# Kernel optimization log

Hardware: AMD Instinct MI355X
Metric: run time of the kernel (lower is better)

The kernel has to match this reference:

```python
import jax, jax.numpy as jnp
import numpy as np

T, B, D, H, OUT = 128, 256, 512, 768, 60


def setup_inputs() -> dict:
    key = jax.random.key(0)
    ks = jax.random.split(key, 8)
    def xavier(k, shape):
        fan_out, fan_in = shape
        limit = np.sqrt(6.0 / (fan_in + fan_out))
        return jax.random.uniform(k, shape, jnp.float32, -limit, limit)
    inp = {
        "input_sample": jax.random.normal(ks[0], (T, B, D), jnp.float32),
        # PyTorch LSTMCell params: weight_ih (4H, D), weight_hh (4H, H), biases (4H,)
        "W_ih": xavier(ks[1], (4 * H, D)),
        "W_hh": xavier(ks[2], (4 * H, H)),
        "b_ih": jax.random.uniform(ks[3], (4 * H,), jnp.float32, -1 / np.sqrt(H), 1 / np.sqrt(H)),
        "b_hh": jax.random.uniform(ks[4], (4 * H,), jnp.float32, -1 / np.sqrt(H), 1 / np.sqrt(H)),
        "W_fc": xavier(ks[5], (OUT, H)),
        "b_fc": jnp.zeros((OUT,), jnp.float32),
    }
    return inp


def _lstm_head(input_sample, W_ih, W_hh, b_ih, b_hh, W_fc, b_fc):
    B_ = input_sample.shape[1]
    H_ = W_hh.shape[1]
    # Precompute input projections for all time steps in one GEMM: (T, B, 4H)
    x_proj = jnp.einsum("tbd,gd->tbg", input_sample, W_ih) + b_ih + b_hh

    def step(carry, xp_t):
        h, c = carry
        gates = xp_t + h @ W_hh.T  # (B, 4H)
        i, f, g, o = jnp.split(gates, 4, axis=-1)  # PyTorch gate order: i, f, g, o
        i = jax.nn.sigmoid(i)
        f = jax.nn.sigmoid(f)
        g = jnp.tanh(g)
        o = jax.nn.sigmoid(o)
        c_new = f * c + i * g
        h_new = o * jnp.tanh(c_new)
        return (h_new, c_new), None

    h0 = jnp.zeros((B_, H_), input_sample.dtype)
    c0 = jnp.zeros((B_, H_), input_sample.dtype)
    (h_T, _), _ = jax.lax.scan(step, (h0, c0), x_proj)
    return h_T @ W_fc.T + b_fc  # (B, OUT)


def reference(input_sample, W_ih, W_hh, b_ih, b_hh, W_fc, b_fc):
    return _lstm_head(input_sample, W_ih, W_hh, b_ih, b_hh, W_fc, b_fc)
```

## Files before the change

kernel.cpp:

```cpp
#include <hip/hip_runtime.h>
#include <stdint.h>

#define T_ 128
#define B_ 256
#define D_ 512
#define H_ 768
#define NG 3072
#define OUT_ 60

using bf16x8 = __attribute__((ext_vector_type(8))) __bf16;
using f32x4  = __attribute__((ext_vector_type(4))) float;
using u32x4  = __attribute__((ext_vector_type(4))) unsigned int;

#define OFF_XB   ((size_t)0)
#define OFF_WI   (OFF_XB + (size_t)T_*B_*D_*2)
#define OFF_WHPK (OFF_WI + (size_t)NG*D_*2)
#define OFF_H    (OFF_WHPK + (size_t)NG*H_*2)
#define OFF_HT   (OFF_H + (size_t)2*B_*H_*2)
#define OFF_BAR  (OFF_HT + (size_t)B_*H_*4)
#define OFF_XP   (OFF_BAR + 65536)
#define OFF_END  (OFF_XP + (size_t)T_*B_*NG*2)

__device__ __forceinline__ unsigned short f2bf(float f) {
  union { float f; unsigned u; } v; v.f = f;
  unsigned r = (v.u + 0x7fffu + ((v.u >> 16) & 1u)) >> 16;
  return (unsigned short)r;
}
__device__ __forceinline__ float sigf(float x) {
  return __builtin_amdgcn_rcpf(1.0f + __expf(-x));
}
__device__ __forceinline__ float tanhf_(float x) {
  return 2.0f * __builtin_amdgcn_rcpf(1.0f + __expf(-2.0f * x)) - 1.0f;
}
__device__ __forceinline__ void gload16(const void* g, void* l) {
  __builtin_amdgcn_global_load_lds(
      (const __attribute__((address_space(1))) unsigned int*)g,
      (__attribute__((address_space(3))) unsigned int*)l, 16, 0, 0);
}
template<int OFF, bool SC1>
__device__ __forceinline__ u32x4 ld16(const void* p) {
  u32x4 r;
  if constexpr (SC1)
    asm volatile("global_load_dwordx4 %0, %1, off offset:%c2 sc0 sc1"
                 : "=v"(r) : "v"(p), "i"(OFF) : "memory");
  else
    asm volatile("global_load_dwordx4 %0, %1, off offset:%c2 sc0"
                 : "=v"(r) : "v"(p), "i"(OFF) : "memory");
  return r;
}
__device__ __forceinline__ unsigned ld4coh(const unsigned* p) {
  unsigned r;
  asm volatile("global_load_dword %0, %1, off sc0 sc1\n\ts_waitcnt vmcnt(0)"
               : "=v"(r) : "v"(p) : "memory");
  return r;
}
template<bool SC1>
__device__ __forceinline__ void st2(ushort* p, unsigned v) {
  if constexpr (SC1)
    asm volatile("global_store_short %0, %1, off sc0 sc1" :: "v"(p), "v"(v) : "memory");
  else
    asm volatile("global_store_short %0, %1, off sc0" :: "v"(p), "v"(v) : "memory");
}
__device__ __forceinline__ void st4coh(unsigned* p, unsigned v) {
  asm volatile("global_store_dword %0, %1, off sc0 sc1" :: "v"(p), "v"(v) : "memory");
}

__global__ void prep_kernel(const float* __restrict__ x,
                            const float* __restrict__ wihf,
                            const float* __restrict__ whhf,
                            uint8_t* __restrict__ ws) {
  ushort* xb = (ushort*)(ws + OFF_XB);
  ushort* wi = (ushort*)(ws + OFF_WI);
  ushort* whpk = (ushort*)(ws + OFF_WHPK);
  unsigned* bar = (unsigned*)(ws + OFF_BAR);
  const size_t tid = (size_t)blockIdx.x * blockDim.x + threadIdx.x;
  const size_t nth = (size_t)gridDim.x * blockDim.x;

  for (size_t i = tid; i < (size_t)T_*B_*D_/4; i += nth) {
    float4 v = ((const float4*)x)[i];
    ushort4 o; o.x=f2bf(v.x); o.y=f2bf(v.y); o.z=f2bf(v.z); o.w=f2bf(v.w);
    ((ushort4*)xb)[i] = o;
  }
  for (size_t i = tid; i < (size_t)NG*D_/4; i += nth) {
    float4 v = ((const float4*)wihf)[i];
    ushort4 o; o.x=f2bf(v.x); o.y=f2bf(v.y); o.z=f2bf(v.z); o.w=f2bf(v.w);
    ((ushort4*)wi)[i] = o;
  }
  for (size_t c = tid; c < (size_t)294912; c += nth) {
    const unsigned L = (unsigned)c & 63u;
    const unsigned r1 = (unsigned)(c >> 6);
    const unsigned nt = r1 % 6u, r2 = r1 / 6u;
    const unsigned kf = r2 % 24u, s = r2 / 24u;
    const unsigned i = nt*16u + (L & 15u);
    const unsigned G = (i & 3u)*768u + s*24u + (i >> 2);
    const unsigned k0 = kf*32u + (L >> 4)*8u;
    const float4 v0 = *(const float4*)(whhf + (size_t)G*768u + k0);
    const float4 v1 = *(const float4*)(whhf + (size_t)G*768u + k0 + 4);
    ushort4 o0, o1;
    o0.x=f2bf(v0.x); o0.y=f2bf(v0.y); o0.z=f2bf(v0.z); o0.w=f2bf(v0.w);
    o1.x=f2bf(v1.x); o1.y=f2bf(v1.y); o1.z=f2bf(v1.z); o1.w=f2bf(v1.w);
    *(ushort4*)(whpk + c*8)     = o0;
    *(ushort4*)(whpk + c*8 + 4) = o1;
  }
  for (size_t i = tid; i < 16384; i += nth) st4coh(&bar[i], 0u);
}

__global__ __launch_bounds__(256) void xproj_kernel(uint8_t* __restrict__ ws) {
  const ushort* __restrict__ xb = (const ushort*)(ws + OFF_XB);
  const ushort* __restrict__ wi = (const ushort*)(ws + OFF_WI);
  ushort* __restrict__ xp = (ushort*)(ws + OFF_XP);

  __shared__ ushort smA[128*64];
  __shared__ ushort smB[128*64];

  const int tid = threadIdx.x;
  const int lane = tid & 63;
  const int w = tid >> 6;
  const int bn = blockIdx.x % 24;
  const int bm = blockIdx.x / 24;
  const int m0 = bm * 128, n0 = bn * 128;
  const int mi = (w >> 1) * 64, ni = (w & 1) * 64;

  f32x4 acc[4][4] = {};

  for (int k0 = 0; k0 < D_; k0 += 64) {
    __syncthreads();
    #pragma unroll
    for (int i = 0; i < 4; ++i) {
      const int ig = w*4 + i;
      const int o  = ig*1024 + lane*16;
      const int row = o >> 7;
      const int colB = o & 127;
      const int scol = colB ^ ((row & 7) << 4);
      gload16((const uint8_t*)xb + ((size_t)(m0+row)*D_ + k0)*2 + scol,
              (uint8_t*)smA + ig*1024);
      gload16((const uint8_t*)wi + ((size_t)(n0+row)*D_ + k0)*2 + scol,
              (uint8_t*)smB + ig*1024);
    }
    __syncthreads();
    #pragma unroll
    for (int kk = 0; kk < 2; ++kk) {
      const int colB = kk*64 + (lane >> 4)*16;
      bf16x8 a[4], b[4];
      #pragma unroll
      for (int mt = 0; mt < 4; ++mt) {
        const int row = mi + mt*16 + (lane & 15);
        a[mt] = *(const bf16x8*)((const uint8_t*)smA + row*128 + (colB ^ ((row & 7) << 4)));
      }
      #pragma unroll
      for (int nt = 0; nt < 4; ++nt) {
        const int row = ni + nt*16 + (lane & 15);
        b[nt] = *(const bf16x8*)((const uint8_t*)smB + row*128 + (colB ^ ((row & 7) << 4)));
      }
      #pragma unroll
      for (int mt = 0; mt < 4; ++mt)
        #pragma unroll
        for (int nt = 0; nt < 4; ++nt)
          acc[mt][nt] = __builtin_amdgcn_mfma_f32_16x16x32_bf16(a[mt], b[nt], acc[mt][nt], 0, 0, 0);
    }
  }
  #pragma unroll
  for (int mt = 0; mt < 4; ++mt)
    #pragma unroll
    for (int nt = 0; nt < 4; ++nt) {
      const int r0 = m0 + mi + mt*16 + (lane >> 4)*4;
      const int c  = n0 + ni + nt*16 + (lane & 15);
      #pragma unroll
      for (int r = 0; r < 4; ++r)
        xp[(size_t)(r0 + r)*NG + c] = f2bf(acc[mt][nt][r]);
    }
}

template<bool SC1>
__device__ __forceinline__ void run_loop(uint8_t* ws, const ushort* whh_lds, float* gbuf,
                                         const float* bih, const float* bhh,
                                         int tid, int g, int s) {
  const int lane = tid & 63, w = tid >> 6, wq = w & 1, wm = w >> 1;
  const int l15 = lane & 15, hi = lane >> 4;
  ushort* hb = (ushort*)(ws + OFF_H);
  const ushort* xp = (const ushort*)(ws + OFF_XP);
  float* hT = (float*)(ws + OFF_HT);
  unsigned* bar = (unsigned*)(ws + OFF_BAR);
  float* gw = gbuf + w*816;

  float bias[3][4];
  #pragma unroll
  for (int j = 0; j < 3; ++j) {
    const int col = s*24 + wq*12 + hi + 4*j;
    #pragma unroll
    for (int q = 0; q < 4; ++q) bias[j][q] = bih[q*H_ + col] + bhh[q*H_ + col];
  }
  const int pl = (lane < 32) ? lane : 31;
  const unsigned* fp = bar + (size_t)(g*32 + pl) * 16;

  const ushort* xpb = xp + (size_t)(g*32 + wm*16 + l15)*NG + s*24 + wq*12 + hi;
  ushort xq[12];
  {
    const ushort* p = xpb;
    #pragma unroll
    for (int q = 0; q < 4; ++q)
      #pragma unroll
      for (int j = 0; j < 3; ++j)
        xq[q*3+j] = p[q*768 + 4*j];
  }

  float cc[3] = {0.f, 0.f, 0.f};

  #pragma unroll 1
  for (int t = 0; t < T_; ++t) {
    f32x4 acc[3] = {};
    if (t > 0) {
      while (1) {
        const unsigned v = ld4coh(fp);
        if (__all((int)(v >= (unsigned)t))) break;
        __builtin_amdgcn_s_sleep(1);
      }
      const ushort* hr = hb + ((size_t)(t & 1)*8 + g)*((size_t)32*H_)
                         + (size_t)(wm*16 + l15)*H_ + hi*8;
      u32x4 ah[24];
      #define LH(i) ah[i] = ld16<(i)*64, SC1>(hr)
      LH(0); LH(1); LH(2); LH(3); LH(4); LH(5); LH(6); LH(7);
      LH(8); LH(9); LH(10); LH(11); LH(12); LH(13); LH(14); LH(15);
      LH(16); LH(17); LH(18); LH(19); LH(20); LH(21); LH(22); LH(23);
      #undef LH
      asm volatile("s_waitcnt vmcnt(0)" ::: "memory");
      __builtin_amdgcn_sched_barrier(0);
      #pragma unroll
      for (int kf = 0; kf < 24; ++kf) {
        const bf16x8 a = *(const bf16x8*)&ah[kf];
        #pragma unroll
        for (int n = 0; n < 3; ++n) {
          const bf16x8 b = *(const bf16x8*)(whh_lds + (size_t)((kf*6 + wq*3 + n)*64 + lane)*8);
          acc[n] = __builtin_amdgcn_mfma_f32_16x16x32_bf16(a, b, acc[n], 0, 0, 0);
        }
      }
    }
    #pragma unroll
    for (int n = 0; n < 3; ++n)
      #pragma unroll
      for (int r = 0; r < 4; ++r)
        gw[(n*16 + l15)*17 + hi*4 + r] = acc[n][r];
    float hv[3];
    #pragma unroll
    for (int j = 0; j < 3; ++j) {
      const int cl = hi + 4*j;
      float gq[4];
      #pragma unroll
      for (int q = 0; q < 4; ++q) {
        union { unsigned u; float f; } xv; xv.u = ((unsigned)xq[q*3 + j]) << 16;
        gq[q] = gw[(cl*4+q)*17 + l15] + xv.f + bias[j][q];
      }
      const float iv = sigf(gq[0]);
      const float fv = sigf(gq[1]);
      const float gv = tanhf_(gq[2]);
      const float ov = sigf(gq[3]);
      const float cn = fv*cc[j] + iv*gv;
      cc[j] = cn;
      hv[j] = ov * tanhf_(cn);
    }
    const int rowl = wm*16 + l15;
    if (t == T_-1) {
      #pragma unroll
      for (int j = 0; j < 3; ++j) {
        const int col = s*24 + wq*12 + hi + 4*j;
        hT[(size_t)(g*32 + rowl)*H_ + col] = hv[j];
      }
      break;
    }
    ushort* hn = hb + ((size_t)((t+1) & 1)*8 + g)*((size_t)32*H_);
    #pragma unroll
    for (int j = 0; j < 3; ++j) {
      const int col = s*24 + wq*12 + hi + 4*j;
      st2<SC1>(hn + (size_t)rowl*H_ + col, (unsigned)f2bf(hv[j]));
    }
    asm volatile("s_waitcnt vmcnt(0)" ::: "memory");
    __syncthreads();
    if (tid == 0) st4coh(bar + (size_t)(g*32 + s)*16, (unsigned)(t + 1));
    {
      const ushort* p = xpb + (size_t)(t + 1)*B_*NG;
      #pragma unroll
      for (int q = 0; q < 4; ++q)
        #pragma unroll
        for (int j = 0; j < 3; ++j)
          xq[q*3+j] = p[q*768 + 4*j];
    }
  }
}

__global__ __launch_bounds__(256, 1) void lstm_kernel(uint8_t* __restrict__ ws,
                                                      const float* __restrict__ bih,
                                                      const float* __restrict__ bhh) {
  __shared__ ushort whh_lds[73728];
  __shared__ float gbuf[3264];
  const int tid = threadIdx.x, lane = tid & 63, w = tid >> 6;
  const int g = blockIdx.x & 7, s = blockIdx.x >> 3;
  unsigned* bar = (unsigned*)(ws + OFF_BAR);

  const uint8_t* wsrc = ws + OFF_WHPK + (size_t)s*9216*16;
  #pragma unroll
  for (int i = 0; i < 36; ++i) {
    const int cb = (w*36 + i)*64;
    gload16(wsrc + (size_t)(cb + lane)*16, (uint8_t*)whh_lds + (size_t)cb*16);
  }

  const unsigned xcd = __builtin_amdgcn_s_getreg((3 << 11) | 20) & 7u;
  if (tid == 0) {
    st4coh(bar + 4096 + blockIdx.x, xcd);
    asm volatile("s_waitcnt vmcnt(0)" ::: "memory");
    __hip_atomic_fetch_add(bar + 5120, 1u, __ATOMIC_RELAXED, __HIP_MEMORY_SCOPE_SYSTEM);
    while (__hip_atomic_load(bar + 5120, __ATOMIC_RELAXED, __HIP_MEMORY_SCOPE_SYSTEM) < 256u)
      __builtin_amdgcn_s_sleep(2);
  }
  __syncthreads();
  const int pl = (lane < 32) ? lane : 31;
  const unsigned oxcc = ld4coh(bar + 4096 + g + 8*pl);
  const bool local = __all((int)(oxcc == xcd));

  asm volatile("s_waitcnt vmcnt(0) lgkmcnt(0)" ::: "memory");
  __syncthreads();

  if (local) run_loop<false>(ws, whh_lds, gbuf, bih, bhh, tid, g, s);
  else       run_loop<true >(ws, whh_lds, gbuf, bih, bhh, tid, g, s);
}

__global__ __launch_bounds__(64) void fc_kernel(const uint8_t* __restrict__ ws,
                                                const float* __restrict__ wfc,
                                                const float* __restrict__ bfc,
                                                float* __restrict__ out) {
  const float* hT = (const float*)(ws + OFF_HT);
  const int b = blockIdx.x;
  const int lane = threadIdx.x;
  const float* hr = hT + (size_t)b*H_;
  float hv[12];
  #pragma unroll
  for (int i = 0; i < 12; ++i) hv[i] = hr[lane + i*64];
  for (int o = 0; o < OUT_; ++o) {
    const float* wr = wfc + (size_t)o*H_;
    float sum = 0.f;
    #pragma unroll
    for (int i = 0; i < 12; ++i) sum += hv[i] * wr[lane + i*64];
    #pragma unroll
    for (int off = 32; off; off >>= 1) sum += __shfl_xor(sum, off);
    if (lane == 0) out[(size_t)b*OUT_ + o] = sum + bfc[o];
  }
}

extern "C" void kernel_launch(void* const* d_in, const int* in_sizes, int n_in,
                              void* d_out, int out_size, void* d_ws, size_t ws_size,
                              hipStream_t stream) {
  const float* x   = (const float*)d_in[0];
  const float* wih = (const float*)d_in[1];
  const float* whh = (const float*)d_in[2];
  const float* bih = (const float*)d_in[3];
  const float* bhh = (const float*)d_in[4];
  const float* wfc = (const float*)d_in[5];
  const float* bfc = (const float*)d_in[6];
  uint8_t* ws = (uint8_t*)d_ws;
  float* out = (float*)d_out;

  prep_kernel<<<dim3(2048), dim3(256), 0, stream>>>(x, wih, whh, ws);
  xproj_kernel<<<dim3(256*24), dim3(256), 0, stream>>>(ws);
  lstm_kernel<<<dim3(256), dim3(256), 0, stream>>>(ws, bih, bhh);
  fc_kernel<<<dim3(256), dim3(64), 0, stream>>>(ws, wfc, bfc, out);
}
```

Baseline: 985.9 us.

## Interleave two independent 16-row batch streams per block in the LSTM recurrence

Each persistent block now handles two 16-row batch groups instead of one 32-row group, and alternates between them every timestep. While one stream waits on its cross-block flag, the other can proceed, which is meant to hide the inter-block synchronisation and h-load latency on the serial critical path. Barrier and h-buffer indexing are reorganised for 16 groups, and the XCD-locality table is moved to a new offset. In exchange, the six gate tiles are split unevenly over four waves, so two waves do redundant MFMA work, and each step performs more MFMA issues and two separate barrier waits.

```diff
diff --git a/kernel.cpp b/kernel.cpp
--- a/kernel.cpp
+++ b/kernel.cpp
@@ -172,118 +172,132 @@
 }
 
 template<bool SC1>
-__device__ __forceinline__ void run_loop(uint8_t* ws, const ushort* whh_lds, float* gbuf,
-                                         const float* bih, const float* bhh,
-                                         int tid, int g, int s) {
-  const int lane = tid & 63, w = tid >> 6, wq = w & 1, wm = w >> 1;
-  const int l15 = lane & 15, hi = lane >> 4;
+__device__ __forceinline__ void stream_slot(
+    uint8_t* __restrict__ ws, const ushort* __restrict__ whh_lds, float* gw,
+    unsigned* __restrict__ bar, int t, int g, int s,
+    int tid, int lane, int l15, int hi,
+    int nt0, int nt1, bool s1store,
+    const float bias[2][4], const int colj[2],
+    ushort xq[8], float cc[2])
+{
   ushort* hb = (ushort*)(ws + OFF_H);
   const ushort* xp = (const ushort*)(ws + OFF_XP);
   float* hT = (float*)(ws + OFF_HT);
+
+  f32x4 acc0 = {0.f,0.f,0.f,0.f}, acc1 = {0.f,0.f,0.f,0.f};
+  if (t > 0) {
+    const int pl = (lane < 32) ? lane : 31;
+    const unsigned* fp = bar + (size_t)(g*32 + pl) * 16;
+    while (1) {
+      const unsigned v = ld4coh(fp);
+      if (__all((int)(v >= (unsigned)t))) break;
+      __builtin_amdgcn_s_sleep(1);
+    }
+    const ushort* hr = hb + ((size_t)(t & 1)*16 + g)*((size_t)16*H_)
+                       + (size_t)l15*H_ + hi*8;
+    u32x4 ah[24];
+    #define LH(i) ah[i] = ld16<(i)*64, SC1>(hr)
+    LH(0); LH(1); LH(2); LH(3); LH(4); LH(5); LH(6); LH(7);
+    LH(8); LH(9); LH(10); LH(11); LH(12); LH(13); LH(14); LH(15);
+    LH(16); LH(17); LH(18); LH(19); LH(20); LH(21); LH(22); LH(23);
+    #undef LH
+    asm volatile("s_waitcnt vmcnt(0)" ::: "memory");
+    __builtin_amdgcn_sched_barrier(0);
+    #pragma unroll
+    for (int kf = 0; kf < 24; ++kf) {
+      const bf16x8 a = *(const bf16x8*)&ah[kf];
+      const bf16x8 b0 = *(const bf16x8*)(whh_lds + (size_t)((kf*6 + nt0)*64 + lane)*8);
+      acc0 = __builtin_amdgcn_mfma_f32_16x16x32_bf16(a, b0, acc0, 0, 0, 0);
+      const bf16x8 b1 = *(const bf16x8*)(whh_lds + (size_t)((kf*6 + nt1)*64 + lane)*8);
+      acc1 = __builtin_amdgcn_mfma_f32_16x16x32_bf16(a, b1, acc1, 0, 0, 0);
+    }
+  }
+  #pragma unroll
+  for (int r = 0; r < 4; ++r) {
+    gw[(size_t)l15*17 + hi*4 + r] = acc0[r];
+    gw[(size_t)(16 + l15)*17 + hi*4 + r] = acc1[r];
+  }
+  float hv[2];
+  #pragma unroll
+  for (int jj = 0; jj < 2; ++jj) {
+    float gq[4];
+    #pragma unroll
+    for (int q = 0; q < 4; ++q) {
+      union { unsigned u; float f; } xv; xv.u = ((unsigned)xq[jj*4 + q]) << 16;
+      gq[q] = gw[(size_t)(jj*16 + hi*4 + q)*17 + l15] + xv.f + bias[jj][q];
+    }
+    const float iv = sigf(gq[0]);
+    const float fv = sigf(gq[1]);
+    const float gv = tanhf_(gq[2]);
+    const float ov = sigf(gq[3]);
+    const float cn = fv*cc[jj] + iv*gv;
+    cc[jj] = cn;
+    hv[jj] = ov * tanhf_(cn);
+  }
+  if (t == T_-1) {
+    hT[(size_t)(g*16 + l15)*H_ + colj[0]] = hv[0];
+    if (s1store) hT[(size_t)(g*16 + l15)*H_ + colj[1]] = hv[1];
+    return;
+  }
+  ushort* hn = hb + ((size_t)((t+1) & 1)*16 + g)*((size_t)16*H_);
+  st2<SC1>(hn + (size_t)l15*H_ + colj[0], (unsigned)f2bf(hv[0]));
+  if (s1store) st2<SC1>(hn + (size_t)l15*H_ + colj[1], (unsigned)f2bf(hv[1]));
+  asm volatile("s_waitcnt vmcnt(0)" ::: "memory");
+  __syncthreads();
+  if (tid == 0) st4coh(bar + (size_t)(g*32 + s)*16, (unsigned)(t + 1));
+  {
+    const ushort* p = xp + ((size_t)(t + 1)*B_ + g*16 + l15)*NG;
+    #pragma unroll
+    for (int jj = 0; jj < 2; ++jj)
+      #pragma unroll
+      for (int q = 0; q < 4; ++q)
+        xq[jj*4 + q] = p[q*H_ + colj[jj]];
+  }
+}
+
+template<bool SC1>
+__device__ __forceinline__ void run_loop(uint8_t* ws, const ushort* whh_lds, float* gbuf,
+                                         const float* bih, const float* bhh,
+                                         int tid, int x, int s) {
+  const int lane = tid & 63, w = tid >> 6;
+  const int l15 = lane & 15, hi = lane >> 4;
   unsigned* bar = (unsigned*)(ws + OFF_BAR);
-  float* gw = gbuf + w*816;
-
-  float bias[3][4];
-  #pragma unroll
-  for (int j = 0; j < 3; ++j) {
-    const int col = s*24 + wq*12 + hi + 4*j;
-    #pragma unroll
-    for (int q = 0; q < 4; ++q) bias[j][q] = bih[q*H_ + col] + bhh[q*H_ + col];
-  }
-  const int pl = (lane < 32) ? lane : 31;
-  const unsigned* fp = bar + (size_t)(g*32 + pl) * 16;
-
-  const ushort* xpb = xp + (size_t)(g*32 + wm*16 + l15)*NG + s*24 + wq*12 + hi;
-  ushort xq[12];
+  const ushort* xp = (const ushort*)(ws + OFF_XP);
+  float* gw = gbuf + w*544;
+
+  const int nt0 = w;
+  const int nt1 = (w < 2) ? (w + 4) : w;
+  const bool s1store = (w < 2);
+  const int colj[2] = { s*24 + nt0*4 + hi, s*24 + nt1*4 + hi };
+
+  float bias[2][4];
+  #pragma unroll
+  for (int jj = 0; jj < 2; ++jj)
+    #pragma unroll
+    for (int q = 0; q < 4; ++q)
+      bias[jj][q] = bih[q*H_ + colj[jj]] + bhh[q*H_ + colj[jj]];
+
+  const int gA = x*2, gB = x*2 + 1;
+  ushort xqA[8], xqB[8];
+  float ccA[2] = {0.f, 0.f}, ccB[2] = {0.f, 0.f};
   {
-    const ushort* p = xpb;
-    #pragma unroll
-    for (int q = 0; q < 4; ++q)
-      #pragma unroll
-      for (int j = 0; j < 3; ++j)
-        xq[q*3+j] = p[q*768 + 4*j];
-  }
-
-  float cc[3] = {0.f, 0.f, 0.f};
+    const ushort* pA = xp + ((size_t)gA*16 + l15)*NG;
+    const ushort* pB = xp + ((size_t)gB*16 + l15)*NG;
+    #pragma unroll
+    for (int jj = 0; jj < 2; ++jj)
+      #pragma unroll
+      for (int q = 0; q < 4; ++q) {
+        xqA[jj*4 + q] = pA[q*H_ + colj[jj]];
+        xqB[jj*4 + q] = pB[q*H_ + colj[jj]];
+      }
+  }
 
   #pragma unroll 1
   for (int t = 0; t < T_; ++t) {
-    f32x4 acc[3] = {};
-    if (t > 0) {
-      while (1) {
-        const unsigned v = ld4coh(fp);
-        if (__all((int)(v >= (unsigned)t))) break;
-        __builtin_amdgcn_s_sleep(1);
-      }
-      const ushort* hr = hb + ((size_t)(t & 1)*8 + g)*((size_t)32*H_)
-                         + (size_t)(wm*16 + l15)*H_ + hi*8;
-      u32x4 ah[24];
-      #define LH(i) ah[i] = ld16<(i)*64, SC1>(hr)
-      LH(0); LH(1); LH(2); LH(3); LH(4); LH(5); LH(6); LH(7);
-      LH(8); LH(9); LH(10); LH(11); LH(12); LH(13); LH(14); LH(15);
-      LH(16); LH(17); LH(18); LH(19); LH(20); LH(21); LH(22); LH(23);
-      #undef LH
-      asm volatile("s_waitcnt vmcnt(0)" ::: "memory");
-      __builtin_amdgcn_sched_barrier(0);
-      #pragma unroll
-      for (int kf = 0; kf < 24; ++kf) {
-        const bf16x8 a = *(const bf16x8*)&ah[kf];
-        #pragma unroll
-        for (int n = 0; n < 3; ++n) {
-          const bf16x8 b = *(const bf16x8*)(whh_lds + (size_t)((kf*6 + wq*3 + n)*64 + lane)*8);
-          acc[n] = __builtin_amdgcn_mfma_f32_16x16x32_bf16(a, b, acc[n], 0, 0, 0);
-        }
-      }
-    }
-    #pragma unroll
-    for (int n = 0; n < 3; ++n)
-      #pragma unroll
-      for (int r = 0; r < 4; ++r)
-        gw[(n*16 + l15)*17 + hi*4 + r] = acc[n][r];
-    float hv[3];
-    #pragma unroll
-    for (int j = 0; j < 3; ++j) {
-      const int cl = hi + 4*j;
-      float gq[4];
-      #pragma unroll
-      for (int q = 0; q < 4; ++q) {
-        union { unsigned u; float f; } xv; xv.u = ((unsigned)xq[q*3 + j]) << 16;
-        gq[q] = gw[(cl*4+q)*17 + l15] + xv.f + bias[j][q];
-      }
-      const float iv = sigf(gq[0]);
-      const float fv = sigf(gq[1]);
-      const float gv = tanhf_(gq[2]);
-      const float ov = sigf(gq[3]);
-      const float cn = fv*cc[j] + iv*gv;
-      cc[j] = cn;
-      hv[j] = ov * tanhf_(cn);
-    }
-    const int rowl = wm*16 + l15;
-    if (t == T_-1) {
-      #pragma unroll
-      for (int j = 0; j < 3; ++j) {
-        const int col = s*24 + wq*12 + hi + 4*j;
-        hT[(size_t)(g*32 + rowl)*H_ + col] = hv[j];
-      }
-      break;
-    }
-    ushort* hn = hb + ((size_t)((t+1) & 1)*8 + g)*((size_t)32*H_);
-    #pragma unroll
-    for (int j = 0; j < 3; ++j) {
-      const int col = s*24 + wq*12 + hi + 4*j;
-      st2<SC1>(hn + (size_t)rowl*H_ + col, (unsigned)f2bf(hv[j]));
-    }
-    asm volatile("s_waitcnt vmcnt(0)" ::: "memory");
-    __syncthreads();
-    if (tid == 0) st4coh(bar + (size_t)(g*32 + s)*16, (unsigned)(t + 1));
-    {
-      const ushort* p = xpb + (size_t)(t + 1)*B_*NG;
-      #pragma unroll
-      for (int q = 0; q < 4; ++q)
-        #pragma unroll
-        for (int j = 0; j < 3; ++j)
-          xq[q*3+j] = p[q*768 + 4*j];
-    }
+    stream_slot<SC1>(ws, whh_lds, gw, bar, t, gA, s, tid, lane, l15, hi,
+                     nt0, nt1, s1store, bias, colj, xqA, ccA);
+    stream_slot<SC1>(ws, whh_lds, gw, bar, t, gB, s, tid, lane, l15, hi,
+                     nt0, nt1, s1store, bias, colj, xqB, ccB);
   }
 }
 
@@ -291,9 +305,9 @@
                                                       const float* __restrict__ bih,
                                                       const float* __restrict__ bhh) {
   __shared__ ushort whh_lds[73728];
-  __shared__ float gbuf[3264];
+  __shared__ float gbuf[2176];
   const int tid = threadIdx.x, lane = tid & 63, w = tid >> 6;
-  const int g = blockIdx.x & 7, s = blockIdx.x >> 3;
+  const int x = blockIdx.x & 7, s = blockIdx.x >> 3;
   unsigned* bar = (unsigned*)(ws + OFF_BAR);
 
   const uint8_t* wsrc = ws + OFF_WHPK + (size_t)s*9216*16;
@@ -305,22 +319,22 @@
 
   const unsigned xcd = __builtin_amdgcn_s_getreg((3 << 11) | 20) & 7u;
   if (tid == 0) {
-    st4coh(bar + 4096 + blockIdx.x, xcd);
+    st4coh(bar + 8192 + blockIdx.x, xcd);
     asm volatile("s_waitcnt vmcnt(0)" ::: "memory");
-    __hip_atomic_fetch_add(bar + 5120, 1u, __ATOMIC_RELAXED, __HIP_MEMORY_SCOPE_SYSTEM);
-    while (__hip_atomic_load(bar + 5120, __ATOMIC_RELAXED, __HIP_MEMORY_SCOPE_SYSTEM) < 256u)
+    __hip_atomic_fetch_add(bar + 8704, 1u, __ATOMIC_RELAXED, __HIP_MEMORY_SCOPE_SYSTEM);
+    while (__hip_atomic_load(bar + 8704, __ATOMIC_RELAXED, __HIP_MEMORY_SCOPE_SYSTEM) < 256u)
       __builtin_amdgcn_s_sleep(2);
   }
   __syncthreads();
   const int pl = (lane < 32) ? lane : 31;
-  const unsigned oxcc = ld4coh(bar + 4096 + g + 8*pl);
+  const unsigned oxcc = ld4coh(bar + 8192 + x + 8*pl);
   const bool local = __all((int)(oxcc == xcd));
 
   asm volatile("s_waitcnt vmcnt(0) lgkmcnt(0)" ::: "memory");
   __syncthreads();
 
-  if (local) run_loop<false>(ws, whh_lds, gbuf, bih, bhh, tid, g, s);
-  else       run_loop<true >(ws, whh_lds, gbuf, bih, bhh, tid, g, s);
+  if (local) run_loop<false>(ws, whh_lds, gbuf, bih, bhh, tid, x, s);
+  else       run_loop<true >(ws, whh_lds, gbuf, bih, bhh, tid, x, s);
 }
 
 __global__ __launch_bounds__(64) void fc_kernel(const uint8_t* __restrict__ ws,
```

Result: slower. 1.513 ms (+53.5%).
